# Optimization experiments

Hardware: AMD Instinct MI355X
Metric: run time of the kernel (lower is better)

## Reference

```python
import jax, jax.numpy as jnp
import numpy as np

GROUP = 128               # group_size
SCALE = float(np.sqrt(GROUP))  # self._scale = sqrt(group_size)
M, N, T = 4096, 4096, 512  # out_features, in_features, tokens


def _rotation(seed: int, n: int) -> jnp.ndarray:
    """Seeded random orthogonal rotation via QR (rotation='qr')."""
    g = np.random.default_rng(seed)
    q, _ = np.linalg.qr(g.standard_normal((n, n)))
    return jnp.asarray(q.astype(np.float32))


def setup_inputs() -> dict:
    key = jax.random.key(0)
    ks = jax.random.split(key, 7)
    x = jax.random.normal(ks[0], (T, N), jnp.float32)
    Pi = _rotation(42, N)    # pass-1 rotation seed (default _rotation_seed = 42)
    Pi2 = _rotation(43, N)   # pass-2 rotation seed
    indices_packed = jax.random.randint(ks[1], (M, N // 2), 0, 256, jnp.int32)
    weight_norms = jax.random.uniform(ks[2], (M, N // GROUP), jnp.float32, 0.5, 1.5)
    codebook = jnp.sort(jax.random.normal(ks[3], (16,), jnp.float32))  # Lloyd-Max centroids
    pass2_indices_packed = jax.random.randint(ks[4], (M, N // 2), 0, 256, jnp.int32)
    pass2_weight_norms = jax.random.uniform(ks[5], (M, N // GROUP), jnp.float32, 0.05, 0.15)
    pass2_codebook = jnp.sort(jax.random.normal(ks[6], (16,), jnp.float32)) * 0.1
    return {
        'x': x, 'Pi': Pi,
        'indices_packed': indices_packed, 'weight_norms': weight_norms, 'codebook': codebook,
        'pass2_indices_packed': pass2_indices_packed, 'pass2_weight_norms': pass2_weight_norms,
        'pass2_codebook': pass2_codebook, 'Pi2': Pi2,
    }


def _dequant(indices_packed, weight_norms, codebook):
    """Unpack 4-bit indices, gather centroids, apply per-group norm scaling.

    indices_packed: (M, N//2) int (uint8 values), low nibble = even column.
    Returns dequantized weight W of shape (M, N).
    """
    low = indices_packed & 0xF
    high = (indices_packed >> 4) & 0xF
    idx = jnp.stack([low, high], axis=-1).reshape(indices_packed.shape[0], -1)  # (M, N)
    w = codebook[idx]                                        # (M, N) centroid gather
    scale = jnp.repeat(weight_norms * (1.0 / SCALE), GROUP, axis=1)  # (M, N)
    return w * scale


def reference(x, Pi, indices_packed, weight_norms, codebook,
              pass2_indices_packed, pass2_weight_norms, pass2_codebook, Pi2):
    # Pass 1: rotate input, multiply by dequantized weight
    W1 = _dequant(indices_packed, weight_norms, codebook)       # (M, N)
    out = (x @ Pi.T) @ W1.T                                     # (T, M)
    # Pass 2 (residual): independent rotation + dequantized residual weight
    W2 = _dequant(pass2_indices_packed, pass2_weight_norms, pass2_codebook)
    out = out + (x @ Pi2.T) @ W2.T
    return out
```

## Files before the change

kernel.cpp:

```cpp
#include <hip/hip_runtime.h>
#include <hip/hip_bf16.h>


typedef __bf16 bf16x8 __attribute__((ext_vector_type(8)));
typedef float  f32x4  __attribute__((ext_vector_type(4)));

#define T_DIM   512
#define N_DIM   4096
#define M_DIM   4096
#define K2_DIM  8192
#define INV_SQRT_G 0.08838834764831843f

typedef const __attribute__((address_space(1))) unsigned int as1_u32;
typedef __attribute__((address_space(3)))       unsigned int as3_u32;

__device__ __forceinline__ void gload16(const void* g, void* l) {
    __builtin_amdgcn_global_load_lds((as1_u32*)g, (as3_u32*)l, 16, 0, 0);
}

__global__ __launch_bounds__(256) void cvt_x_kernel(
    const float* __restrict__ x, __bf16* __restrict__ xb)
{
    int i = (blockIdx.x * 256 + threadIdx.x) * 8;
    float4 f0 = *(const float4*)&x[i];
    float4 f1 = *(const float4*)&x[i + 4];
    bf16x8 h = { (__bf16)f0.x, (__bf16)f0.y, (__bf16)f0.z, (__bf16)f0.w,
                 (__bf16)f1.x, (__bf16)f1.y, (__bf16)f1.z, (__bf16)f1.w };
    *(bf16x8*)&xb[i] = h;
}

__global__ __launch_bounds__(256) void cvt_y_kernel(
    const float* __restrict__ Y32, __bf16* __restrict__ Y)
{
    int i = (blockIdx.x * 256 + threadIdx.x) * 8;
    float4 f0 = *(const float4*)&Y32[i];
    float4 f1 = *(const float4*)&Y32[i + 4];
    bf16x8 h = { (__bf16)f0.x, (__bf16)f0.y, (__bf16)f0.z, (__bf16)f0.w,
                 (__bf16)f1.x, (__bf16)f1.y, (__bf16)f1.z, (__bf16)f1.w };
    *(bf16x8*)&Y[i] = h;
}

template<bool SPLITK>
__global__ __launch_bounds__(256, 3) void gemm1_kernel(
    const __bf16* __restrict__ xb, const float* __restrict__ Pi,
    const float* __restrict__ Pi2, float* __restrict__ Y32,
    __bf16* __restrict__ Y)
{
    __shared__ __bf16 sA[2][128 * 32];
    __shared__ __bf16 sB[2][128 * 32];

    const int tid   = threadIdx.x;
    const int n0    = blockIdx.x * 128;
    const int t0    = blockIdx.y * 128;
    const int kbase = blockIdx.z * (SPLITK ? 1024 : N_DIM);
    const int NK    = (SPLITK ? 1024 : N_DIM) / 32;

    const float* Bsrc = (n0 < N_DIM) ? Pi : Pi2;
    const int nloc = n0 & (N_DIM - 1);

    const int wid = tid >> 6, lane = tid & 63;
    const int wr = (wid >> 1) * 64, wc = (wid & 1) * 64;
    const int lr = lane & 15, lg = lane >> 4;
    const int sw = lr & 3;

    const int arow = wid * 16 + (lane >> 2);
    const int acol = (lane & 3) * 8;
    const int br = tid >> 1, bh = tid & 1;

    f32x4 acc[4][4] = {};
    float4 rb[4];

    auto issueA = [&](int buf, int k0) {
        #pragma unroll
        for (int c = 0; c < 2; ++c)
            gload16(&xb[(size_t)(t0 + c * 64 + arow) * N_DIM + k0 + acol],
                    &sA[buf][(c * 64 + wid * 16) * 32]);
    };
    auto loadB = [&](int k0) {
        const float* bp = &Bsrc[(size_t)(nloc + br) * N_DIM + k0 + bh * 16];
        #pragma unroll
        for (int q = 0; q < 4; ++q) rb[q] = *(const float4*)(bp + q * 4);
    };
    auto writeB = [&](int buf) {
        #pragma unroll
        for (int h = 0; h < 2; ++h) {
            float4 f0 = rb[h * 2], f1 = rb[h * 2 + 1];
            bf16x8 v = { (__bf16)f0.x, (__bf16)f0.y, (__bf16)f0.z, (__bf16)f0.w,
                         (__bf16)f1.x, (__bf16)f1.y, (__bf16)f1.z, (__bf16)f1.w };
            int unit = (bh * 2 + h) ^ (br & 3);
            *(bf16x8*)&sB[buf][br * 32 + unit * 8] = v;
        }
    };

    loadB(kbase);
    issueA(0, kbase);
    writeB(0);
    __syncthreads();

    int cur = 0;
    for (int k = 0; k < NK; ++k) {
        const int kn = kbase + (k + 1) * 32;
        if (k + 1 < NK) { loadB(kn); issueA(cur ^ 1, kn); }

        bf16x8 af[4], bf[4];
        #pragma unroll
        for (int m = 0; m < 4; ++m)
            af[m] = *(const bf16x8*)&sA[cur][(wr + m * 16 + lr) * 32 + lg * 8];
        #pragma unroll
        for (int n = 0; n < 4; ++n)
            bf[n] = *(const bf16x8*)&sB[cur][(wc + n * 16 + lr) * 32 + (lg ^ sw) * 8];
        #pragma unroll
        for (int m = 0; m < 4; ++m)
            #pragma unroll
            for (int n = 0; n < 4; ++n)
                acc[m][n] = __builtin_amdgcn_mfma_f32_16x16x32_bf16(
                    af[m], bf[n], acc[m][n], 0, 0, 0);

        if (k + 1 < NK) writeB(cur ^ 1);
        __syncthreads();
        cur ^= 1;
    }

    #pragma unroll
    for (int m = 0; m < 4; ++m)
        #pragma unroll
        for (int n = 0; n < 4; ++n)
            #pragma unroll
            for (int e = 0; e < 4; ++e) {
                size_t off = (size_t)(t0 + wr + m * 16 + lg * 4 + e) * K2_DIM +
                             n0 + wc + n * 16 + lr;
                if (SPLITK) unsafeAtomicAdd(&Y32[off], acc[m][n][e]);
                else        Y[off] = (__bf16)acc[m][n][e];
            }
}

__global__ __launch_bounds__(256, 3) void gemm2_kernel(
    const __bf16* __restrict__ Y,
    const int*   __restrict__ idx1, const float* __restrict__ wn1,
    const float* __restrict__ cb1,
    const int*   __restrict__ idx2, const float* __restrict__ wn2,
    const float* __restrict__ cb2,
    float* __restrict__ out)
{
    __shared__ __bf16 sA[2][128 * 32];
    __shared__ __bf16 sB[2][128 * 32];
    __shared__ float2 lut[256];

    const int tid  = threadIdx.x;
    const int m0   = blockIdx.x * 128;
    const int t0   = blockIdx.y * 128;
    const int pass = blockIdx.z >> 2;
    const int kof  = (blockIdx.z & 3) * 1024;

    const int*   idxp = pass ? idx2 : idx1;
    const float* wn   = pass ? wn2  : wn1;
    const float* cbg  = pass ? cb2  : cb1;

    lut[tid] = make_float2(cbg[tid & 15] * INV_SQRT_G,
                           cbg[(tid >> 4) & 15] * INV_SQRT_G);

    const int wid = tid >> 6, lane = tid & 63;
    const int wr = (wid >> 1) * 64, wc = (wid & 1) * 64;
    const int lr = lane & 15, lg = lane >> 4;
    const int sw = lr & 3;

    const int arow = wid * 16 + (lane >> 2);
    const int acol = (lane & 3) * 8;
    const int br = tid >> 1, bh = tid & 1;

    f32x4 acc[4][4] = {};
    int4  wi[2];
    float wscale;

    auto issueA = [&](int buf, int kl) {
        #pragma unroll
        for (int c = 0; c < 2; ++c)
            gload16(&Y[(size_t)(t0 + c * 64 + arow) * K2_DIM + pass * N_DIM + kl + acol],
                    &sA[buf][(c * 64 + wid * 16) * 32]);
    };
    auto loadB = [&](int kl) {
        const int* ip = &idxp[(size_t)(m0 + br) * (N_DIM / 2) + (kl >> 1) + bh * 8];
        wi[0] = *(const int4*)ip;
        wi[1] = *(const int4*)(ip + 4);
        wscale = wn[(size_t)(m0 + br) * 32 + (kl >> 7)];
    };
    auto writeB = [&](int buf) {
        #pragma unroll
        for (int h = 0; h < 2; ++h) {
            int4 v = wi[h];
            float2 p0 = lut[v.x & 255], p1 = lut[v.y & 255];
            float2 p2 = lut[v.z & 255], p3 = lut[v.w & 255];
            bf16x8 w = { (__bf16)(p0.x * wscale), (__bf16)(p0.y * wscale),
                         (__bf16)(p1.x * wscale), (__bf16)(p1.y * wscale),
                         (__bf16)(p2.x * wscale), (__bf16)(p2.y * wscale),
                         (__bf16)(p3.x * wscale), (__bf16)(p3.y * wscale) };
            int unit = (bh * 2 + h) ^ (br & 3);
            *(bf16x8*)&sB[buf][br * 32 + unit * 8] = w;
        }
    };

    loadB(kof);
    issueA(0, kof);
    __syncthreads();
    writeB(0);
    __syncthreads();

    int cur = 0;
    const int NK = 1024 / 32;
    for (int k = 0; k < NK; ++k) {
        const int kn = kof + (k + 1) * 32;
        if (k + 1 < NK) { loadB(kn); issueA(cur ^ 1, kn); }

        bf16x8 af[4], bf[4];
        #pragma unroll
        for (int m = 0; m < 4; ++m)
            af[m] = *(const bf16x8*)&sA[cur][(wr + m * 16 + lr) * 32 + lg * 8];
        #pragma unroll
        for (int n = 0; n < 4; ++n)
            bf[n] = *(const bf16x8*)&sB[cur][(wc + n * 16 + lr) * 32 + (lg ^ sw) * 8];
        #pragma unroll
        for (int m = 0; m < 4; ++m)
            #pragma unroll
            for (int n = 0; n < 4; ++n)
                acc[m][n] = __builtin_amdgcn_mfma_f32_16x16x32_bf16(
                    af[m], bf[n], acc[m][n], 0, 0, 0);

        if (k + 1 < NK) writeB(cur ^ 1);
        __syncthreads();
        cur ^= 1;
    }

    #pragma unroll
    for (int m = 0; m < 4; ++m)
        #pragma unroll
        for (int n = 0; n < 4; ++n)
            #pragma unroll
            for (int e = 0; e < 4; ++e)
                unsafeAtomicAdd(&out[(size_t)(t0 + wr + m * 16 + lg * 4 + e) * M_DIM +
                                     m0 + wc + n * 16 + lr], acc[m][n][e]);
}

extern "C" void kernel_launch(void* const* d_in, const int* in_sizes, int n_in,
                              void* d_out, int out_size, void* d_ws, size_t ws_size,
                              hipStream_t stream) {
    const float* x    = (const float*)d_in[0];
    const float* Pi   = (const float*)d_in[1];
    const int*   idx1 = (const int*)  d_in[2];
    const float* wn1  = (const float*)d_in[3];
    const float* cb1  = (const float*)d_in[4];
    const int*   idx2 = (const int*)  d_in[5];
    const float* wn2  = (const float*)d_in[6];
    const float* cb2  = (const float*)d_in[7];
    const float* Pi2  = (const float*)d_in[8];
    float* out = (float*)d_out;

    const size_t xb_bytes  = (size_t)T_DIM * N_DIM * sizeof(__bf16);
    const size_t y32_bytes = (size_t)T_DIM * K2_DIM * sizeof(float);
    const size_t y_bytes   = (size_t)T_DIM * K2_DIM * sizeof(__bf16);
    const bool   splitk    = ws_size >= xb_bytes + y32_bytes + y_bytes;

    __bf16* xb  = (__bf16*)d_ws;
    float*  Y32 = (float*)((char*)d_ws + xb_bytes);
    __bf16* Yb  = splitk ? (__bf16*)((char*)d_ws + xb_bytes + y32_bytes)
                         : (__bf16*)((char*)d_ws + xb_bytes);

    hipMemsetAsync(out, 0, (size_t)T_DIM * M_DIM * sizeof(float), stream);
    cvt_x_kernel<<<dim3(T_DIM * N_DIM / (256 * 8)), dim3(256), 0, stream>>>(x, xb);

    if (splitk) {
        hipMemsetAsync(Y32, 0, y32_bytes, stream);
        gemm1_kernel<true><<<dim3(K2_DIM / 128, T_DIM / 128, 4), dim3(256), 0, stream>>>(
            xb, Pi, Pi2, Y32, Yb);
        cvt_y_kernel<<<dim3(T_DIM * K2_DIM / (256 * 8)), dim3(256), 0, stream>>>(Y32, Yb);
    } else {
        gemm1_kernel<false><<<dim3(K2_DIM / 128, T_DIM / 128, 1), dim3(256), 0, stream>>>(
            xb, Pi, Pi2, Y32, Yb);
    }

    gemm2_kernel<<<dim3(M_DIM / 128, T_DIM / 128, 8), dim3(256), 0, stream>>>(
        Yb, idx1, wn1, cb1, idx2, wn2, cb2, out);
}
```

Measured before the change: 379.3 us.

## Pre-dequantize weights and pre-convert rotations to bf16 before generic NT GEMMs

Adds a dequant kernel that writes both passes' weights as one concatenated bf16 matrix, plus a kernel that converts Pi and Pi2 to bf16 up front. Both GEMMs then run through a generic NT kernel that loads A and B directly into LDS asynchronously, with no in-loop conversion or LUT gathers. The goal is to take fp32-to-bf16 conversion and LUT dequant off the GEMM inner loops. The cost is extra full passes over the weight and rotation matrices through HBM and a much larger workspace. The older fused kernels are kept as fallbacks when the workspace is too small.

```diff
diff --git a/kernel.cpp b/kernel.cpp
--- a/kernel.cpp
+++ b/kernel.cpp
@@ -40,8 +40,126 @@
     *(bf16x8*)&Y[i] = h;
 }
 
+__global__ __launch_bounds__(256) void cvt_rot_kernel(
+    const float* __restrict__ Pi, const float* __restrict__ Pi2,
+    __bf16* __restrict__ Pib)
+{
+    size_t i = ((size_t)blockIdx.x * 256 + threadIdx.x) * 8;
+    const size_t half = (size_t)N_DIM * N_DIM;
+    const float* src = (i < half) ? (Pi + i) : (Pi2 + (i - half));
+    float4 f0 = *(const float4*)src;
+    float4 f1 = *(const float4*)(src + 4);
+    bf16x8 h = { (__bf16)f0.x, (__bf16)f0.y, (__bf16)f0.z, (__bf16)f0.w,
+                 (__bf16)f1.x, (__bf16)f1.y, (__bf16)f1.z, (__bf16)f1.w };
+    *(bf16x8*)&Pib[i] = h;
+}
+
+__global__ __launch_bounds__(256) void dequant_kernel(
+    const int*   __restrict__ idx1, const float* __restrict__ wn1,
+    const float* __restrict__ cb1,
+    const int*   __restrict__ idx2, const float* __restrict__ wn2,
+    const float* __restrict__ cb2,
+    __bf16* __restrict__ Wcat)
+{
+    __shared__ float2 lut[2][256];
+    const int t = threadIdx.x;
+    lut[0][t] = make_float2(cb1[t & 15] * INV_SQRT_G, cb1[(t >> 4) & 15] * INV_SQRT_G);
+    lut[1][t] = make_float2(cb2[t & 15] * INV_SQRT_G, cb2[(t >> 4) & 15] * INV_SQRT_G);
+    __syncthreads();
+
+    const int f  = blockIdx.x * 256 + t;
+    const int m  = f >> 9;
+    const int jb = f & 511;
+    const int pass = jb >> 8;
+    const int jl = (jb & 255) * 16;
+
+    const int* ip = (pass ? idx2 : idx1) + (size_t)m * (N_DIM / 2) + (jl >> 1);
+    const float ws = (pass ? wn2 : wn1)[m * 32 + (jl >> 7)];
+    const float2* L = lut[pass];
+
+    int4 v0 = *(const int4*)ip;
+    int4 v1 = *(const int4*)(ip + 4);
+    auto dq8 = [&](int4 v) -> bf16x8 {
+        float2 p0 = L[v.x & 255], p1 = L[v.y & 255];
+        float2 p2 = L[v.z & 255], p3 = L[v.w & 255];
+        bf16x8 w = { (__bf16)(p0.x * ws), (__bf16)(p0.y * ws),
+                     (__bf16)(p1.x * ws), (__bf16)(p1.y * ws),
+                     (__bf16)(p2.x * ws), (__bf16)(p2.y * ws),
+                     (__bf16)(p3.x * ws), (__bf16)(p3.y * ws) };
+        return w;
+    };
+    __bf16* dst = &Wcat[(size_t)m * K2_DIM + jb * 16];
+    *(bf16x8*)dst       = dq8(v0);
+    *(bf16x8*)(dst + 8) = dq8(v1);
+}
+
+__global__ __launch_bounds__(256, 3) void gemm_nt_kernel(
+    const __bf16* __restrict__ A, const __bf16* __restrict__ B,
+    float* __restrict__ C, int lda, int ldb, int ldc)
+{
+    __shared__ __bf16 sA[2][128 * 32];
+    __shared__ __bf16 sB[2][128 * 32];
+
+    const int tid = threadIdx.x;
+    const int n0  = blockIdx.x * 128;
+    const int m0  = blockIdx.y * 128;
+    const int k0  = blockIdx.z * 1024;
+
+    const int wid = tid >> 6, lane = tid & 63;
+    const int wr = (wid >> 1) * 64, wc = (wid & 1) * 64;
+    const int lr = lane & 15, lg = lane >> 4;
+    const int srow = lane >> 2, sunit = lane & 3;
+
+    f32x4 acc[4][4] = {};
+
+    auto issue = [&](int buf, int kk) {
+        #pragma unroll
+        for (int i = 0; i < 2; ++i) {
+            const int c = wid * 2 + i;
+            gload16(&A[(size_t)(m0 + c * 16 + srow) * lda + kk + sunit * 8],
+                    &sA[buf][c * 512]);
+            gload16(&B[(size_t)(n0 + c * 16 + srow) * ldb + kk + sunit * 8],
+                    &sB[buf][c * 512]);
+        }
+    };
+
+    issue(0, k0);
+    __syncthreads();
+
+    int cur = 0;
+    for (int k = 0; k < 32; ++k) {
+        if (k + 1 < 32) issue(cur ^ 1, k0 + (k + 1) * 32);
+
+        bf16x8 af[4], bf[4];
+        #pragma unroll
+        for (int m = 0; m < 4; ++m)
+            af[m] = *(const bf16x8*)&sA[cur][(wr + m * 16 + lr) * 32 + lg * 8];
+        #pragma unroll
+        for (int n = 0; n < 4; ++n)
+            bf[n] = *(const bf16x8*)&sB[cur][(wc + n * 16 + lr) * 32 + lg * 8];
+        #pragma unroll
+        for (int m = 0; m < 4; ++m)
+            #pragma unroll
+            for (int n = 0; n < 4; ++n)
+                acc[m][n] = __builtin_amdgcn_mfma_f32_16x16x32_bf16(
+                    af[m], bf[n], acc[m][n], 0, 0, 0);
+
+        __syncthreads();
+        cur ^= 1;
+    }
+
+    #pragma unroll
+    for (int m = 0; m < 4; ++m)
+        #pragma unroll
+        for (int n = 0; n < 4; ++n)
+            #pragma unroll
+            for (int e = 0; e < 4; ++e)
+                unsafeAtomicAdd(&C[(size_t)(m0 + wr + m * 16 + lg * 4 + e) * ldc +
+                                   n0 + wc + n * 16 + lr], acc[m][n][e]);
+}
+
 template<bool SPLITK>
-__global__ __launch_bounds__(256, 3) void gemm1_kernel(
+__global__ __launch_bounds__(256, 3) void gemm1_fb_kernel(
     const __bf16* __restrict__ xb, const float* __restrict__ Pi,
     const float* __restrict__ Pi2, float* __restrict__ Y32,
     __bf16* __restrict__ Y)
@@ -92,9 +210,7 @@
         }
     };
 
-    loadB(kbase);
-    issueA(0, kbase);
-    writeB(0);
+    loadB(kbase); issueA(0, kbase); writeB(0);
     __syncthreads();
 
     int cur = 0;
@@ -134,7 +250,7 @@
             }
 }
 
-__global__ __launch_bounds__(256, 3) void gemm2_kernel(
+__global__ __launch_bounds__(256, 3) void gemm2_fb_kernel(
     const __bf16* __restrict__ Y,
     const int*   __restrict__ idx1, const float* __restrict__ wn1,
     const float* __restrict__ cb1,
@@ -199,8 +315,7 @@
         }
     };
 
-    loadB(kof);
-    issueA(0, kof);
+    loadB(kof); issueA(0, kof);
     __syncthreads();
     writeB(0);
     __syncthreads();
@@ -254,29 +369,48 @@
     const float* Pi2  = (const float*)d_in[8];
     float* out = (float*)d_out;
 
-    const size_t xb_bytes  = (size_t)T_DIM * N_DIM * sizeof(__bf16);
-    const size_t y32_bytes = (size_t)T_DIM * K2_DIM * sizeof(float);
-    const size_t y_bytes   = (size_t)T_DIM * K2_DIM * sizeof(__bf16);
-    const bool   splitk    = ws_size >= xb_bytes + y32_bytes + y_bytes;
-
-    __bf16* xb  = (__bf16*)d_ws;
-    float*  Y32 = (float*)((char*)d_ws + xb_bytes);
-    __bf16* Yb  = splitk ? (__bf16*)((char*)d_ws + xb_bytes + y32_bytes)
-                         : (__bf16*)((char*)d_ws + xb_bytes);
+    const size_t MB = 1024ull * 1024ull;
+    __bf16* xb   = (__bf16*)d_ws;
+    float*  Y32  = (float*) ((char*)d_ws + 4  * MB);
+    __bf16* Ybf  = (__bf16*)((char*)d_ws + 20 * MB);
+    __bf16* Wcat = (__bf16*)((char*)d_ws + 28 * MB);
+    __bf16* Pib  = (__bf16*)((char*)d_ws + 92 * MB);
+
+    const bool fullT = ws_size >= 156 * MB;
+    const bool midT  = ws_size >= 92 * MB;
+    const bool lowT  = ws_size >= 28 * MB;
 
     hipMemsetAsync(out, 0, (size_t)T_DIM * M_DIM * sizeof(float), stream);
     cvt_x_kernel<<<dim3(T_DIM * N_DIM / (256 * 8)), dim3(256), 0, stream>>>(x, xb);
 
-    if (splitk) {
-        hipMemsetAsync(Y32, 0, y32_bytes, stream);
-        gemm1_kernel<true><<<dim3(K2_DIM / 128, T_DIM / 128, 4), dim3(256), 0, stream>>>(
-            xb, Pi, Pi2, Y32, Yb);
-        cvt_y_kernel<<<dim3(T_DIM * K2_DIM / (256 * 8)), dim3(256), 0, stream>>>(Y32, Yb);
+    if (midT)
+        dequant_kernel<<<dim3(M_DIM * (K2_DIM / 16) / 256), dim3(256), 0, stream>>>(
+            idx1, wn1, cb1, idx2, wn2, cb2, Wcat);
+
+    if (fullT) {
+        cvt_rot_kernel<<<dim3(2 * N_DIM * N_DIM / (256 * 8)), dim3(256), 0, stream>>>(
+            Pi, Pi2, Pib);
+        hipMemsetAsync(Y32, 0, 16 * MB, stream);
+        gemm_nt_kernel<<<dim3(K2_DIM / 128, T_DIM / 128, 4), dim3(256), 0, stream>>>(
+            xb, Pib, Y32, N_DIM, N_DIM, K2_DIM);
+        cvt_y_kernel<<<dim3(T_DIM * K2_DIM / (256 * 8)), dim3(256), 0, stream>>>(Y32, Ybf);
+    } else if (lowT) {
+        hipMemsetAsync(Y32, 0, 16 * MB, stream);
+        gemm1_fb_kernel<true><<<dim3(K2_DIM / 128, T_DIM / 128, 4), dim3(256), 0, stream>>>(
+            xb, Pi, Pi2, Y32, Ybf);
+        cvt_y_kernel<<<dim3(T_DIM * K2_DIM / (256 * 8)), dim3(256), 0, stream>>>(Y32, Ybf);
     } else {
-        gemm1_kernel<false><<<dim3(K2_DIM / 128, T_DIM / 128, 1), dim3(256), 0, stream>>>(
-            xb, Pi, Pi2, Y32, Yb);
+        __bf16* Ytiny = (__bf16*)((char*)d_ws + 4 * MB);
+        gemm1_fb_kernel<false><<<dim3(K2_DIM / 128, T_DIM / 128, 1), dim3(256), 0, stream>>>(
+            xb, Pi, Pi2, Y32, Ytiny);
+        Ybf = Ytiny;
     }
 
-    gemm2_kernel<<<dim3(M_DIM / 128, T_DIM / 128, 8), dim3(256), 0, stream>>>(
-        Yb, idx1, wn1, cb1, idx2, wn2, cb2, out);
-}
+    if (midT) {
+        gemm_nt_kernel<<<dim3(M_DIM / 128, T_DIM / 128, 8), dim3(256), 0, stream>>>(
+            Ybf, Wcat, out, K2_DIM, K2_DIM, M_DIM);
+    } else {
+        gemm2_fb_kernel<<<dim3(M_DIM / 128, T_DIM / 128, 8), dim3(256), 0, stream>>>(
+            Ybf, idx1, wn1, cb1, idx2, wn2, cb2, out);
+    }
+}
```

Measured after the change: 411.7 us. +8.5%, slower.
